# Kernel tuning notes

Hardware: AMD Instinct MI355X
Metric: run time of the kernel (lower is better)

The kernel has to match this reference:

```python
import jax, jax.numpy as jnp
import numpy as np

K = 4        # num_instances per identity
MARGIN = 0.3

def setup_inputs() -> dict:
    key = jax.random.key(0)
    n, d = 4096, 2048
    inputs = jax.random.normal(key, (n, d), dtype=jnp.float32)
    # PK-sampled labels: K consecutive instances share a class id
    targets = jnp.arange(n, dtype=jnp.int32) // K
    epoch = 0  # unused by the loss, kept for signature fidelity
    return {"inputs": inputs, "targets": targets, "epoch": epoch}

def reference(inputs, targets, epoch):
    n = inputs.shape[0]
    P = n // K
    # pairwise Euclidean distance matrix (the addmm GEMM)
    sq = jnp.sum(inputs * inputs, axis=1)                      # [n]
    dist = sq[:, None] + sq[None, :] - 2.0 * (inputs @ inputs.T)
    dist = jnp.sqrt(jnp.clip(dist, 1e-12, None))               # [n, n]
    mask = targets[:, None] == targets[None, :]                 # [n, n]
    # semi-hard mining, vectorized over the original triple loop:
    # hardest negative per anchor row
    neg_min = jnp.min(jnp.where(mask, jnp.inf, dist), axis=1)   # [n]
    # within-identity KxK distance blocks: dist[i*K+j, i*K+p]
    within = dist.reshape(P, K, P, K)[jnp.arange(P), :, jnp.arange(P), :]  # [P,K,K]
    jj, pp = jnp.triu_indices(K, k=1)  # row-major order == (j, pair>j) loop order
    dist_ap = within[:, jj, pp].reshape(-1)                     # [P*K*(K-1)/2]
    dist_an = neg_min.reshape(P, K)[:, jj].reshape(-1)          # anchor's hardest neg, repeated per positive
    # MarginRankingLoss(y=1, mean): mean(relu(-(an - ap) + margin))
    loss = jnp.mean(jnp.maximum(dist_ap - dist_an + MARGIN, 0.0))
    prec = jnp.mean((dist_an > dist_ap).astype(jnp.float32))
    return loss, prec
```

## Files before the change

### kernel.cpp

```cpp
#include <hip/hip_runtime.h>
#include <hip/hip_bf16.h>
#include <hip/hip_fp8.h>
#include <stdint.h>


#define N_ROWS 4096
#define DIM    2048
#define P_IDS  1024
#define NPAIR  (P_IDS * 6)
#define MARGIN 0.3f
#define BK     64
#define NT     (DIM / BK)
#define NIT    (NT / 2)
#define NTILE  32
#define NBLK   528

typedef __attribute__((ext_vector_type(4))) float f32x4;
typedef __attribute__((ext_vector_type(2))) long long2v;

__global__ __launch_bounds__(256) void prep_kernel(const float* __restrict__ in,
                                                   uint8_t* __restrict__ f8m,
                                                   float* __restrict__ sq,
                                                   unsigned* __restrict__ neg_bits) {
    const int row = blockIdx.x;
    const int t = threadIdx.x;
    const float4* rp = (const float4*)(in + (size_t)row * DIM);
    float4 v0 = rp[t * 2 + 0];
    float4 v1 = rp[t * 2 + 1];
    float s = v0.x * v0.x + v0.y * v0.y + v0.z * v0.z + v0.w * v0.w
            + v1.x * v1.x + v1.y * v1.y + v1.z * v1.z + v1.w * v1.w;
    unsigned w0 = (unsigned)__builtin_amdgcn_cvt_pk_fp8_f32(v0.x, v0.y, 0, false);
    w0 = (unsigned)__builtin_amdgcn_cvt_pk_fp8_f32(v0.z, v0.w, (int)w0, true);
    unsigned w1 = (unsigned)__builtin_amdgcn_cvt_pk_fp8_f32(v1.x, v1.y, 0, false);
    w1 = (unsigned)__builtin_amdgcn_cvt_pk_fp8_f32(v1.z, v1.w, (int)w1, true);
    const int pos = (t >> 3) * 64 + (t & 3) * 16 + ((t >> 2) & 1) * 8;
    uint2 o; o.x = w0; o.y = w1;
    *(uint2*)(f8m + (size_t)row * DIM + pos) = o;
    #pragma unroll
    for (int m = 32; m; m >>= 1) s += __shfl_down(s, m, 64);
    __shared__ float red[4];
    if ((t & 63) == 0) red[t >> 6] = s;
    __syncthreads();
    if (t == 0) {
        sq[row] = red[0] + red[1] + red[2] + red[3];
        neg_bits[row] = 0x7F800000u;
    }
}

__global__ __launch_bounds__(256, 4) void gemm_kernel(const uint8_t* __restrict__ f8m,
                                                      const float* __restrict__ sq,
                                                      unsigned* __restrict__ neg_bits,
                                                      float* __restrict__ dist_ap) {
    extern __shared__ char smem[];
    uint8_t* const Asb = (uint8_t*)smem;
    uint8_t* const Bsb = (uint8_t*)(smem + 16384);
    #define AS(B,R,C) Asb[((B) << 13) + ((R) << 6) + (C)]
    #define BS(B,R,C) Bsb[((B) << 13) + ((R) << 6) + (C)]

    const int bid = (blockIdx.x & 7) * (NBLK / 8) + (blockIdx.x >> 3);
    int rem = bid, bi = 0;
    while (rem >= NTILE - bi) { rem -= NTILE - bi; ++bi; }
    const int bj = bi + rem;

    const int t = threadIdx.x;
    const int lane = t & 63;
    const int wave = t >> 6;
    const int wr = (wave >> 1) * 64;
    const int wc = (wave & 1) * 64;
    const int lr = lane & 15;
    const int l4 = lane >> 4;
    f32x4 acc[4][4] = {};

    const int rowA0 = bi * 128;
    const int rowB0 = bj * 128;
    const int sr  = lane >> 2;
    const int gg  = (lane & 3) ^ ((lane >> 3) & 3);
    const uint8_t* gA = f8m + (size_t)(rowA0 + sr) * DIM + (gg << 4);
    const uint8_t* gB = f8m + (size_t)(rowB0 + sr) * DIM + (gg << 4);

    #define STAGE_HT(GBASE, LDSB, BUF, KT)                                        \
        { _Pragma("unroll")                                                       \
          for (int g = 0; g < 2; ++g) {                                           \
              const int chunk = wave * 2 + g;                                     \
              __builtin_amdgcn_global_load_lds(                                   \
                  (const __attribute__((address_space(1))) void*)                 \
                      ((GBASE) + (size_t)chunk * 16 * DIM + (KT) * BK),           \
                  (__attribute__((address_space(3))) void*)                       \
                      ((char*)(LDSB) + (BUF) * 8192 + chunk * 1024),              \
                  16, 0, 0);                                                      \
          } }
    #define STAGE_A(BUF, KT) STAGE_HT(gA, Asb, BUF, KT)
    #define STAGE_B(BUF, KT) STAGE_HT(gB, Bsb, BUF, KT)

    long2v afp[2], bfp0[2], bfp1[2];
    #define SLOTCOL ((l4 ^ ((lr >> 1) & 3)) << 4)
    #define LOAD_AF(BUF, MH)                                                      \
        { _Pragma("unroll") for (int m = 0; m < 2; ++m)                           \
              afp[m] = *(const long2v*)&AS(BUF,                                   \
                  wr + ((MH) * 2 + m) * 16 + lr, SLOTCOL); }
    #define LOAD_BF(DST, BUF, NH)                                                 \
        { _Pragma("unroll") for (int n = 0; n < 2; ++n)                           \
              DST[n] = *(const long2v*)&BS(BUF,                                   \
                  wc + ((NH) * 2 + n) * 16 + lr, SLOTCOL); }

    #define MFMA_Q(MH, NH, BF)                                                    \
        { __builtin_amdgcn_s_setprio(1);                                          \
          _Pragma("unroll") for (int ks = 0; ks < 2; ++ks)                        \
          _Pragma("unroll") for (int m = 0; m < 2; ++m)                           \
          _Pragma("unroll") for (int n = 0; n < 2; ++n)                           \
              acc[(MH) * 2 + m][(NH) * 2 + n] =                                   \
                  __builtin_amdgcn_mfma_f32_16x16x32_fp8_fp8(                     \
                      afp[m][ks], BF[n][ks],                                      \
                      acc[(MH) * 2 + m][(NH) * 2 + n], 0, 0, 0);                  \
          __builtin_amdgcn_s_setprio(0); }

    #define BARR() __builtin_amdgcn_s_barrier()
    #define VMW(N) asm volatile("s_waitcnt vmcnt(" #N ")" ::: "memory")

    STAGE_A(0, 0);
    STAGE_B(0, 0);
    STAGE_B(1, 1);
    VMW(0);
    BARR();

    for (int i = 0; i < NIT - 1; ++i) {
        const int t2 = 2 * i;
        LOAD_AF(0, 0); LOAD_BF(bfp0, 0, 0);
        STAGE_A(1, t2 + 1);
        BARR(); MFMA_Q(0, 0, bfp0); BARR();
        LOAD_BF(bfp1, 0, 1);
        BARR(); MFMA_Q(0, 1, bfp1); BARR();
        LOAD_AF(0, 1);
        STAGE_B(0, t2 + 2);
        BARR(); MFMA_Q(1, 1, bfp1); BARR();
        BARR(); MFMA_Q(1, 0, bfp0); VMW(2); BARR();
        LOAD_AF(1, 0); LOAD_BF(bfp0, 1, 0);
        STAGE_A(0, t2 + 2);
        BARR(); MFMA_Q(0, 0, bfp0); BARR();
        LOAD_BF(bfp1, 1, 1);
        BARR(); MFMA_Q(0, 1, bfp1); BARR();
        LOAD_AF(1, 1);
        STAGE_B(1, t2 + 3);
        BARR(); MFMA_Q(1, 1, bfp1); BARR();
        BARR(); MFMA_Q(1, 0, bfp0); VMW(2); BARR();
    }
    {
        LOAD_AF(0, 0); LOAD_BF(bfp0, 0, 0);
        STAGE_A(1, NT - 1);
        BARR(); MFMA_Q(0, 0, bfp0); BARR();
        LOAD_BF(bfp1, 0, 1);
        BARR(); MFMA_Q(0, 1, bfp1); BARR();
        LOAD_AF(0, 1);
        BARR(); MFMA_Q(1, 1, bfp1); BARR();
        BARR(); MFMA_Q(1, 0, bfp0); VMW(0); BARR();
        LOAD_AF(1, 0); LOAD_BF(bfp0, 1, 0);
        BARR(); MFMA_Q(0, 0, bfp0); BARR();
        LOAD_BF(bfp1, 1, 1);
        BARR(); MFMA_Q(0, 1, bfp1); BARR();
        LOAD_AF(1, 1);
        BARR(); MFMA_Q(1, 1, bfp1); BARR();
        MFMA_Q(1, 0, bfp0);
    }

    const bool diag = (bi == bj);
    const int l15 = lane & 15;
    float sqc[4];
    #pragma unroll
    for (int n = 0; n < 4; ++n) sqc[n] = sq[rowB0 + wc + n * 16 + l15];
    float colmin[4] = {INFINITY, INFINITY, INFINITY, INFINITY};

    #pragma unroll
    for (int m = 0; m < 4; ++m) {
        #pragma unroll
        for (int r = 0; r < 4; ++r) {
            const int grow = rowA0 + wr + m * 16 + l4 * 4 + r;
            const float sqr = sq[grow];
            float rmin = INFINITY;
            #pragma unroll
            for (int n = 0; n < 4; ++n) {
                const int gcol = rowB0 + wc + n * 16 + l15;
                const float d2 = sqr + sqc[n] - 2.0f * acc[m][n][r];
                const float d = sqrtf(fmaxf(d2, 1e-12f));
                float cand = d;
                if (diag && ((grow >> 2) == (gcol >> 2))) {
                    if (grow < gcol) {
                        const int p = grow >> 2;
                        const int a = grow & 3, b = gcol & 3;
                        dist_ap[p * 6 + (a * (7 - a)) / 2 + (b - a - 1)] = d;
                    }
                    cand = INFINITY;
                }
                rmin = fminf(rmin, cand);
                colmin[n] = fminf(colmin[n], cand);
            }
            rmin = fminf(rmin, __shfl_xor(rmin, 1, 64));
            rmin = fminf(rmin, __shfl_xor(rmin, 2, 64));
            rmin = fminf(rmin, __shfl_xor(rmin, 4, 64));
            rmin = fminf(rmin, __shfl_xor(rmin, 8, 64));
            if (l15 == 0) atomicMin(&neg_bits[grow], __float_as_uint(rmin));
        }
    }
    if (!diag) {
        #pragma unroll
        for (int n = 0; n < 4; ++n) {
            float v = colmin[n];
            v = fminf(v, __shfl_xor(v, 16, 64));
            v = fminf(v, __shfl_xor(v, 32, 64));
            if (l4 == 0)
                atomicMin(&neg_bits[rowB0 + wc + n * 16 + l15], __float_as_uint(v));
        }
    }
}

__global__ __launch_bounds__(256) void finalize_kernel(const unsigned* __restrict__ neg_bits,
                                                       const float* __restrict__ dist_ap,
                                                       float* __restrict__ out) {
    const int t = threadIdx.x;
    float sum = 0.f, cnt = 0.f;
    for (int e = t; e < NPAIR; e += 256) {
        const int p = e / 6;
        const int idx = e - p * 6;
        const int a = (idx < 3) ? 0 : ((idx < 5) ? 1 : 2);
        const float an = __uint_as_float(neg_bits[p * 4 + a]);
        const float ap = dist_ap[e];
        sum += fmaxf(ap - an + MARGIN, 0.f);
        cnt += (an > ap) ? 1.f : 0.f;
    }
    #pragma unroll
    for (int m = 32; m; m >>= 1) {
        sum += __shfl_down(sum, m, 64);
        cnt += __shfl_down(cnt, m, 64);
    }
    __shared__ float rs[4], rc[4];
    if ((t & 63) == 0) { rs[t >> 6] = sum; rc[t >> 6] = cnt; }
    __syncthreads();
    if (t == 0) {
        out[0] = (rs[0] + rs[1] + rs[2] + rs[3]) / (float)NPAIR;
        out[1] = (rc[0] + rc[1] + rc[2] + rc[3]) / (float)NPAIR;
    }
}

extern "C" void kernel_launch(void* const* d_in, const int* in_sizes, int n_in,
                              void* d_out, int out_size, void* d_ws, size_t ws_size,
                              hipStream_t stream) {
    const float* inputs = (const float*)d_in[0];
    float* out = (float*)d_out;
    char* ws = (char*)d_ws;
    uint8_t* f8m = (uint8_t*)ws;
    float* sq = (float*)(ws + (size_t)N_ROWS * DIM);
    unsigned* neg_bits = (unsigned*)((char*)sq + N_ROWS * 4);
    float* dist_ap = (float*)((char*)neg_bits + N_ROWS * 4);

    prep_kernel<<<N_ROWS, 256, 0, stream>>>(inputs, f8m, sq, neg_bits);
    gemm_kernel<<<NBLK, 256, 32768, stream>>>(f8m, sq, neg_bits, dist_ap);
    finalize_kernel<<<1, 256, 0, stream>>>(neg_bits, dist_ap, out);
}
```

Before: 64.85 us.

## Switch GEMM to single-wave 64x64 tiles with simple double-buffered K loop

Replaces the 4-wave 128x128 block tile with a single-wave 64x64 tile, giving 2080 upper-triangular blocks instead of 528. The barrier-heavy interleaved schedule is replaced by a straightforward double-buffered loop that waits on vmcnt, issues all 32 MFMAs per K-step, then prefetches two steps ahead. The goal is to remove the barriers and raise parallelism across the CUs. The cost is halved operand reuse per tile, so more global and L2 traffic, and more atomicMin operations in the epilogue.

```diff
diff --git a/kernel.cpp b/kernel.cpp
--- a/kernel.cpp
+++ b/kernel.cpp
@@ -11,9 +11,8 @@
 #define MARGIN 0.3f
 #define BK     64
 #define NT     (DIM / BK)
-#define NIT    (NT / 2)
-#define NTILE  32
-#define NBLK   528
+#define NTILE  64
+#define NBLK   2080
 
 typedef __attribute__((ext_vector_type(4))) float f32x4;
 typedef __attribute__((ext_vector_type(2))) long long2v;
@@ -47,138 +46,94 @@
     }
 }
 
-__global__ __launch_bounds__(256, 4) void gemm_kernel(const uint8_t* __restrict__ f8m,
-                                                      const float* __restrict__ sq,
-                                                      unsigned* __restrict__ neg_bits,
-                                                      float* __restrict__ dist_ap) {
+__global__ __launch_bounds__(64, 4) void gemm_kernel(const uint8_t* __restrict__ f8m,
+                                                     const float* __restrict__ sq,
+                                                     unsigned* __restrict__ neg_bits,
+                                                     float* __restrict__ dist_ap) {
     extern __shared__ char smem[];
     uint8_t* const Asb = (uint8_t*)smem;
-    uint8_t* const Bsb = (uint8_t*)(smem + 16384);
-    #define AS(B,R,C) Asb[((B) << 13) + ((R) << 6) + (C)]
-    #define BS(B,R,C) Bsb[((B) << 13) + ((R) << 6) + (C)]
+    uint8_t* const Bsb = (uint8_t*)(smem + 8192);
+    #define AS(B,R,C) Asb[((B) << 12) + ((R) << 6) + (C)]
+    #define BS(B,R,C) Bsb[((B) << 12) + ((R) << 6) + (C)]
 
     const int bid = (blockIdx.x & 7) * (NBLK / 8) + (blockIdx.x >> 3);
     int rem = bid, bi = 0;
     while (rem >= NTILE - bi) { rem -= NTILE - bi; ++bi; }
     const int bj = bi + rem;
 
-    const int t = threadIdx.x;
-    const int lane = t & 63;
-    const int wave = t >> 6;
-    const int wr = (wave >> 1) * 64;
-    const int wc = (wave & 1) * 64;
+    const int lane = threadIdx.x;
     const int lr = lane & 15;
     const int l4 = lane >> 4;
     f32x4 acc[4][4] = {};
 
-    const int rowA0 = bi * 128;
-    const int rowB0 = bj * 128;
+    const int rowA0 = bi * 64;
+    const int rowB0 = bj * 64;
     const int sr  = lane >> 2;
     const int gg  = (lane & 3) ^ ((lane >> 3) & 3);
     const uint8_t* gA = f8m + (size_t)(rowA0 + sr) * DIM + (gg << 4);
     const uint8_t* gB = f8m + (size_t)(rowB0 + sr) * DIM + (gg << 4);
 
-    #define STAGE_HT(GBASE, LDSB, BUF, KT)                                        \
+    #define STAGE_T(GBASE, LDSB, BUF, KT)                                         \
         { _Pragma("unroll")                                                       \
-          for (int g = 0; g < 2; ++g) {                                           \
-              const int chunk = wave * 2 + g;                                     \
+          for (int g = 0; g < 4; ++g) {                                           \
               __builtin_amdgcn_global_load_lds(                                   \
                   (const __attribute__((address_space(1))) void*)                 \
-                      ((GBASE) + (size_t)chunk * 16 * DIM + (KT) * BK),           \
+                      ((GBASE) + (size_t)g * 16 * DIM + (KT) * BK),               \
                   (__attribute__((address_space(3))) void*)                       \
-                      ((char*)(LDSB) + (BUF) * 8192 + chunk * 1024),              \
+                      ((char*)(LDSB) + (BUF) * 4096 + g * 1024),                  \
                   16, 0, 0);                                                      \
           } }
-    #define STAGE_A(BUF, KT) STAGE_HT(gA, Asb, BUF, KT)
-    #define STAGE_B(BUF, KT) STAGE_HT(gB, Bsb, BUF, KT)
-
-    long2v afp[2], bfp0[2], bfp1[2];
+    #define STAGE_A(BUF, KT) STAGE_T(gA, Asb, BUF, KT)
+    #define STAGE_B(BUF, KT) STAGE_T(gB, Bsb, BUF, KT)
+
+    long2v afp[4], bfp[4];
     #define SLOTCOL ((l4 ^ ((lr >> 1) & 3)) << 4)
-    #define LOAD_AF(BUF, MH)                                                      \
-        { _Pragma("unroll") for (int m = 0; m < 2; ++m)                           \
-              afp[m] = *(const long2v*)&AS(BUF,                                   \
-                  wr + ((MH) * 2 + m) * 16 + lr, SLOTCOL); }
-    #define LOAD_BF(DST, BUF, NH)                                                 \
-        { _Pragma("unroll") for (int n = 0; n < 2; ++n)                           \
-              DST[n] = *(const long2v*)&BS(BUF,                                   \
-                  wc + ((NH) * 2 + n) * 16 + lr, SLOTCOL); }
-
-    #define MFMA_Q(MH, NH, BF)                                                    \
-        { __builtin_amdgcn_s_setprio(1);                                          \
-          _Pragma("unroll") for (int ks = 0; ks < 2; ++ks)                        \
-          _Pragma("unroll") for (int m = 0; m < 2; ++m)                           \
-          _Pragma("unroll") for (int n = 0; n < 2; ++n)                           \
-              acc[(MH) * 2 + m][(NH) * 2 + n] =                                   \
-                  __builtin_amdgcn_mfma_f32_16x16x32_fp8_fp8(                     \
-                      afp[m][ks], BF[n][ks],                                      \
-                      acc[(MH) * 2 + m][(NH) * 2 + n], 0, 0, 0);                  \
-          __builtin_amdgcn_s_setprio(0); }
-
-    #define BARR() __builtin_amdgcn_s_barrier()
+
     #define VMW(N) asm volatile("s_waitcnt vmcnt(" #N ")" ::: "memory")
 
-    STAGE_A(0, 0);
-    STAGE_B(0, 0);
-    STAGE_B(1, 1);
-    VMW(0);
-    BARR();
-
-    for (int i = 0; i < NIT - 1; ++i) {
-        const int t2 = 2 * i;
-        LOAD_AF(0, 0); LOAD_BF(bfp0, 0, 0);
-        STAGE_A(1, t2 + 1);
-        BARR(); MFMA_Q(0, 0, bfp0); BARR();
-        LOAD_BF(bfp1, 0, 1);
-        BARR(); MFMA_Q(0, 1, bfp1); BARR();
-        LOAD_AF(0, 1);
-        STAGE_B(0, t2 + 2);
-        BARR(); MFMA_Q(1, 1, bfp1); BARR();
-        BARR(); MFMA_Q(1, 0, bfp0); VMW(2); BARR();
-        LOAD_AF(1, 0); LOAD_BF(bfp0, 1, 0);
-        STAGE_A(0, t2 + 2);
-        BARR(); MFMA_Q(0, 0, bfp0); BARR();
-        LOAD_BF(bfp1, 1, 1);
-        BARR(); MFMA_Q(0, 1, bfp1); BARR();
-        LOAD_AF(1, 1);
-        STAGE_B(1, t2 + 3);
-        BARR(); MFMA_Q(1, 1, bfp1); BARR();
-        BARR(); MFMA_Q(1, 0, bfp0); VMW(2); BARR();
-    }
-    {
-        LOAD_AF(0, 0); LOAD_BF(bfp0, 0, 0);
-        STAGE_A(1, NT - 1);
-        BARR(); MFMA_Q(0, 0, bfp0); BARR();
-        LOAD_BF(bfp1, 0, 1);
-        BARR(); MFMA_Q(0, 1, bfp1); BARR();
-        LOAD_AF(0, 1);
-        BARR(); MFMA_Q(1, 1, bfp1); BARR();
-        BARR(); MFMA_Q(1, 0, bfp0); VMW(0); BARR();
-        LOAD_AF(1, 0); LOAD_BF(bfp0, 1, 0);
-        BARR(); MFMA_Q(0, 0, bfp0); BARR();
-        LOAD_BF(bfp1, 1, 1);
-        BARR(); MFMA_Q(0, 1, bfp1); BARR();
-        LOAD_AF(1, 1);
-        BARR(); MFMA_Q(1, 1, bfp1); BARR();
-        MFMA_Q(1, 0, bfp0);
+    STAGE_A(0, 0); STAGE_B(0, 0);
+    STAGE_A(1, 1); STAGE_B(1, 1);
+
+    for (int kt = 0; kt < NT; ++kt) {
+        const int buf = kt & 1;
+        if (kt == NT - 1) { VMW(0); } else { VMW(8); }
+        #pragma unroll
+        for (int m = 0; m < 4; ++m)
+            afp[m] = *(const long2v*)&AS(buf, m * 16 + lr, SLOTCOL);
+        #pragma unroll
+        for (int n = 0; n < 4; ++n)
+            bfp[n] = *(const long2v*)&BS(buf, n * 16 + lr, SLOTCOL);
+        __builtin_amdgcn_s_setprio(1);
+        #pragma unroll
+        for (int ks = 0; ks < 2; ++ks)
+            #pragma unroll
+            for (int m = 0; m < 4; ++m)
+                #pragma unroll
+                for (int n = 0; n < 4; ++n)
+                    acc[m][n] = __builtin_amdgcn_mfma_f32_16x16x32_fp8_fp8(
+                        afp[m][ks], bfp[n][ks], acc[m][n], 0, 0, 0);
+        __builtin_amdgcn_s_setprio(0);
+        __builtin_amdgcn_sched_barrier(0);
+        if (kt + 2 < NT) { STAGE_A(buf, kt + 2); STAGE_B(buf, kt + 2); }
     }
 
     const bool diag = (bi == bj);
     const int l15 = lane & 15;
     float sqc[4];
     #pragma unroll
-    for (int n = 0; n < 4; ++n) sqc[n] = sq[rowB0 + wc + n * 16 + l15];
+    for (int n = 0; n < 4; ++n) sqc[n] = sq[rowB0 + n * 16 + l15];
     float colmin[4] = {INFINITY, INFINITY, INFINITY, INFINITY};
 
     #pragma unroll
     for (int m = 0; m < 4; ++m) {
         #pragma unroll
         for (int r = 0; r < 4; ++r) {
-            const int grow = rowA0 + wr + m * 16 + l4 * 4 + r;
+            const int grow = rowA0 + m * 16 + l4 * 4 + r;
             const float sqr = sq[grow];
             float rmin = INFINITY;
             #pragma unroll
             for (int n = 0; n < 4; ++n) {
-                const int gcol = rowB0 + wc + n * 16 + l15;
+                const int gcol = rowB0 + n * 16 + l15;
                 const float d2 = sqr + sqc[n] - 2.0f * acc[m][n][r];
                 const float d = sqrtf(fmaxf(d2, 1e-12f));
                 float cand = d;
@@ -207,7 +162,7 @@
             v = fminf(v, __shfl_xor(v, 16, 64));
             v = fminf(v, __shfl_xor(v, 32, 64));
             if (l4 == 0)
-                atomicMin(&neg_bits[rowB0 + wc + n * 16 + l15], __float_as_uint(v));
+                atomicMin(&neg_bits[rowB0 + n * 16 + l15], __float_as_uint(v));
         }
     }
 }
@@ -252,6 +207,6 @@
     float* dist_ap = (float*)((char*)neg_bits + N_ROWS * 4);
 
     prep_kernel<<<N_ROWS, 256, 0, stream>>>(inputs, f8m, sq, neg_bits);
-    gemm_kernel<<<NBLK, 256, 32768, stream>>>(f8m, sq, neg_bits, dist_ap);
+    gemm_kernel<<<NBLK, 64, 16384, stream>>>(f8m, sq, neg_bits, dist_ap);
     finalize_kernel<<<1, 256, 0, stream>>>(neg_bits, dist_ap, out);
 }
```

Result: slower. 75.67 us (+16.7%).
